# Kernel tuning notes

Measured on AMD Instinct MI355X. Metric: run time of the kernel, lower is better.

The kernel has to match this reference:

```python
import jax, jax.numpy as jnp
import numpy as np

BATCH = 4096
LATENT = 2048
ZDIM = 128
TEMP = 0.5
PRIOR = 0.3
PRIOR_PRIME = 0.5
GAMMA = 1.0
BETA = 0.0
EPS = 1e-8  # torch CosineSimilarity eps


def setup_inputs() -> dict:
    key = jax.random.key(0)
    k = jax.random.split(key, 6)
    return {
        "h_i": jax.random.normal(k[0], (BATCH, LATENT), dtype=jnp.float32),
        "h_j": jax.random.normal(k[1], (BATCH, LATENT), dtype=jnp.float32),
        "z_i": jax.random.normal(k[2], (BATCH, ZDIM), dtype=jnp.float32),
        "z_j": jax.random.normal(k[3], (BATCH, ZDIM), dtype=jnp.float32),
        "target": jax.random.randint(k[4], (BATCH, 1), 0, 2, dtype=jnp.int64 if jax.config.jax_enable_x64 else jnp.int32),
        "W": jax.random.normal(k[5], (1, LATENT), dtype=jnp.float32) * (1.0 / np.sqrt(LATENT)),
        "b": jnp.zeros((1,), dtype=jnp.float32),
        "weight_onnpu": jnp.asarray(0.5, dtype=jnp.float32),
    }


def _onnpu_loss(inp, target):
    # inp: [B, 1] classifier logit; target: [B, 1] in {0, 1} -> {-1, +1}
    t = (target * 2 - 1).astype(inp.dtype)
    positive = (t == 1).astype(inp.dtype)
    unlabeled = (t == -1).astype(inp.dtype)
    one = jnp.asarray(1.0, inp.dtype)
    n_pos = jnp.maximum(one, jnp.sum(positive))
    n_unl = jnp.maximum(one, jnp.sum(unlabeled))
    sig = jax.nn.sigmoid  # loss(x) = sigmoid(-x)
    y_pos = sig(-(positive * inp)) * positive
    y_pos_inv = sig(positive * inp) * positive
    y_unl = sig(unlabeled * inp) * unlabeled
    positive_risk = PRIOR_PRIME / n_pos * jnp.sum(y_pos)
    negative_risk = ((1.0 - PRIOR_PRIME) / (n_unl * (1.0 - PRIOR)) * jnp.sum(y_unl)
                     - (1.0 - PRIOR_PRIME) * PRIOR / (n_pos * (1.0 - PRIOR)) * jnp.sum(y_pos_inv))
    # nnPU correction (nnPU=True, beta=0, gamma=1)
    return jnp.where(negative_risk < -BETA, -GAMMA * negative_risk,
                     positive_risk + negative_risk)


def _nt_xent_loss(z_i, z_j):
    B = z_i.shape[0]
    N = 2 * B
    z = jnp.concatenate([z_i, z_j], axis=0)  # [N, D]
    zn = z / jnp.maximum(jnp.linalg.norm(z, axis=1, keepdims=True), EPS)
    sim = (zn @ zn.T) / TEMP  # [N, N] cosine similarity / temperature
    idx = jnp.arange(N)
    pos = sim[idx, (idx + B) % N]  # positive pair logit per row
    # CE over [positive | all-other-than-self]: denominator is logsumexp over
    # the row with the self-similarity (diagonal) excluded.
    sim_masked = jnp.where(idx[:, None] == idx[None, :], -jnp.inf, sim)
    lse = jax.nn.logsumexp(sim_masked, axis=1)
    return jnp.sum(lse - pos) / N


def reference(h_i, h_j, z_i, z_j, target, W, b, weight_onnpu):
    logit_i = h_i @ W.T + b  # [B, 1]
    logit_j = h_j @ W.T + b
    onnpu_l = 0.5 * (_onnpu_loss(logit_i, target) + _onnpu_loss(logit_j, target))
    nt_xent_l = _nt_xent_loss(z_i, z_j)
    return weight_onnpu * onnpu_l + (1.0 - weight_onnpu) * nt_xent_l
```

## Files before the change

kernel.cpp:

```cpp
#include <hip/hip_runtime.h>

#define BATCH  4096
#define NROWS  8192
#define LATENT 2048
#define ZDIM   128
#define PRIORc       0.3f
#define PRIOR_PRIMEc 0.5f

typedef __attribute__((ext_vector_type(8))) short bf16x8;
typedef __attribute__((ext_vector_type(4))) float f32x4;

__device__ inline unsigned short f2bf_rne(float f) {
    unsigned int u = __float_as_uint(f);
    u = u + 0x7fffu + ((u >> 16) & 1u);
    return (unsigned short)(u >> 16);
}

__device__ inline float wave_reduce_sum(float v) {
#pragma unroll
    for (int m = 1; m < 64; m <<= 1) v += __shfl_xor(v, m, 64);
    return v;
}

__global__ void k_zprep(const float* __restrict__ z_i, const float* __restrict__ z_j,
                        unsigned short* __restrict__ znb, float* __restrict__ pos) {
    int wave = threadIdx.x >> 6, lane = threadIdx.x & 63;
    int r = blockIdx.x * 4 + wave;
    int p = r + BATCH;
    float2 a = ((const float2*)(z_i + (size_t)r * ZDIM))[lane];
    float2 c = ((const float2*)(z_j + (size_t)r * ZDIM))[lane];
    float sa = a.x * a.x + a.y * a.y;
    float sc = c.x * c.x + c.y * c.y;
    float dd = a.x * c.x + a.y * c.y;
    sa = wave_reduce_sum(sa);
    sc = wave_reduce_sum(sc);
    dd = wave_reduce_sum(dd);
    float inva = 1.f / fmaxf(sqrtf(sa), 1e-8f);
    float invc = 1.f / fmaxf(sqrtf(sc), 1e-8f);
    if (lane == 0) {
        float pv = 2.0f * dd * inva * invc;
        pos[r] = pv;
        pos[p] = pv;
    }
    int kt = lane >> 4;
    int q  = (lane >> 2) & 3;
    int j  = (lane & 3) * 2;
    int lrow = q * 16;
    float fa = inva * 1.41421356237f, fc = invc * 1.41421356237f;
    {
        size_t off = ((size_t)((r >> 4) * 4 + kt) * 64 + (lrow + (r & 15))) * 8 + j;
        ushort2 w2; w2.x = f2bf_rne(a.x * fa); w2.y = f2bf_rne(a.y * fa);
        *(ushort2*)(znb + off) = w2;
    }
    {
        size_t off = ((size_t)((p >> 4) * 4 + kt) * 64 + (lrow + (p & 15))) * 8 + j;
        ushort2 w2; w2.x = f2bf_rne(c.x * fc); w2.y = f2bf_rne(c.y * fc);
        *(ushort2*)(znb + off) = w2;
    }
}

__global__ void __launch_bounds__(256, 3) k_mega(
        const unsigned short* __restrict__ znb, float* __restrict__ S_row,
        const float* __restrict__ h_i, const float* __restrict__ h_j,
        const float* __restrict__ W, const float* __restrict__ bb,
        float* __restrict__ logits) {
    int bid = blockIdx.x;
    int lane = threadIdx.x & 63, wave = threadIdx.x >> 6;
    if (bid < 1024) {
        int q = lane >> 4, t = lane & 15;
        int row0 = (bid & 63) * 128 + (wave >> 1) * 64;
        int gA = row0 >> 4;
        const bf16x8* zf = (const bf16x8*)znb;

        bf16x8 a[4][4];
#pragma unroll
        for (int mt = 0; mt < 4; ++mt)
#pragma unroll
            for (int kt = 0; kt < 4; ++kt)
                a[mt][kt] = zf[(size_t)((gA + mt) * 4 + kt) * 64 + lane];

        float s[16];
#pragma unroll
        for (int i = 0; i < 16; ++i) s[i] = 0.f;

        int colbase = (bid >> 6) * 512 + (wave & 1) * 64;
        int cb4 = colbase >> 4;
        bf16x8 b[4];
#pragma unroll
        for (int kt = 0; kt < 4; ++kt)
            b[kt] = zf[(size_t)(cb4 * 4 + kt) * 64 + lane];

#pragma unroll 1
        for (int it = 0; it < 4; ++it) {
#pragma unroll
            for (int nt = 0; nt < 4; ++nt) {
                bf16x8 bn[4];
                if (!(it == 3 && nt == 3)) {
                    int ng = cb4 + (nt == 3 ? (it + 1) * 8 : it * 8 + nt + 1);
#pragma unroll
                    for (int kt = 0; kt < 4; ++kt)
                        bn[kt] = zf[(size_t)(ng * 4 + kt) * 64 + lane];
                }
                f32x4 acc[4];
                f32x4 zero = {0.f, 0.f, 0.f, 0.f};
#pragma unroll
                for (int mt = 0; mt < 4; ++mt) acc[mt] = zero;
#pragma unroll
                for (int kt = 0; kt < 4; ++kt)
#pragma unroll
                    for (int mt = 0; mt < 4; ++mt)
                        acc[mt] = __builtin_amdgcn_mfma_f32_16x16x32_bf16(a[mt][kt], b[kt], acc[mt], 0, 0, 0);
                int gcol = colbase + it * 128 + nt * 16 + t;
#pragma unroll
                for (int mt = 0; mt < 4; ++mt) {
                    int rowb = row0 + mt * 16 + q * 4;
#pragma unroll
                    for (int reg = 0; reg < 4; ++reg) {
                        float e = __expf(acc[mt][reg]);
                        s[mt * 4 + reg] += (rowb + reg == gcol) ? 0.f : e;
                    }
                }
#pragma unroll
                for (int kt = 0; kt < 4; ++kt) b[kt] = bn[kt];
            }
        }
#pragma unroll
        for (int i = 0; i < 16; ++i) {
            float v = s[i];
            v += __shfl_xor(v, 1, 64);
            v += __shfl_xor(v, 2, 64);
            v += __shfl_xor(v, 4, 64);
            v += __shfl_xor(v, 8, 64);
            if (t == 0) atomicAdd(&S_row[row0 + (i >> 2) * 16 + q * 4 + (i & 3)], v);
        }
    } else {
        int r = (bid - 1024) * 4 + wave;
        const float* h = (r < BATCH) ? (h_i + (size_t)r * LATENT)
                                     : (h_j + (size_t)(r - BATCH) * LATENT);
        const float4* h4 = (const float4*)h;
        const float4* w4 = (const float4*)W;
        float s = 0.f;
#pragma unroll
        for (int itr = 0; itr < 8; ++itr) {
            float4 av = h4[itr * 64 + lane];
            float4 wv = w4[itr * 64 + lane];
            s += av.x * wv.x + av.y * wv.y + av.z * wv.z + av.w * wv.w;
        }
        s = wave_reduce_sum(s);
        if (lane == 0) logits[r] = s + bb[0];
    }
}

__global__ void k_final(const float* __restrict__ S_row, const float* __restrict__ pos,
                        const float* __restrict__ logits, const int* __restrict__ target,
                        const float* __restrict__ w_onnpu, float* __restrict__ out) {
    float nt_s = 0.f;
    for (int r = threadIdx.x; r < NROWS; r += 1024)
        nt_s += __logf(S_row[r]) - pos[r];
    float v[8];
#pragma unroll
    for (int i = 0; i < 8; ++i) v[i] = 0.f;
    for (int r = threadIdx.x; r < BATCH; r += 1024) {
        float li = logits[r], lj = logits[BATCH + r];
        bool p = (target[r] == 1);
        float si_n = 1.f / (1.f + __expf(li));
        float si_p = 1.f / (1.f + __expf(-li));
        float sj_n = 1.f / (1.f + __expf(lj));
        float sj_p = 1.f / (1.f + __expf(-lj));
        v[0] += p ? 1.f : 0.f;
        v[1] += p ? 0.f : 1.f;
        v[2] += p ? si_n : 0.f;
        v[3] += p ? si_p : 0.f;
        v[4] += p ? 0.f : si_p;
        v[5] += p ? sj_n : 0.f;
        v[6] += p ? sj_p : 0.f;
        v[7] += p ? 0.f : sj_p;
    }
    __shared__ float red[16][9];
    int wave = threadIdx.x >> 6, lane = threadIdx.x & 63;
    nt_s = wave_reduce_sum(nt_s);
#pragma unroll
    for (int i = 0; i < 8; ++i) v[i] = wave_reduce_sum(v[i]);
    if (lane == 0) {
        red[wave][0] = nt_s;
#pragma unroll
        for (int i = 0; i < 8; ++i) red[wave][1 + i] = v[i];
    }
    __syncthreads();
    if (threadIdx.x == 0) {
        float t[9];
#pragma unroll
        for (int i = 0; i < 9; ++i) {
            float acc = 0.f;
#pragma unroll
            for (int wv = 0; wv < 16; ++wv) acc += red[wv][i];
            t[i] = acc;
        }
        float ntxent = t[0] / (float)NROWS;
        float np = fmaxf(1.f, t[1]), nu = fmaxf(1.f, t[2]);
        float pr_i = PRIOR_PRIMEc / np * t[3];
        float nr_i = (1.f - PRIOR_PRIMEc) / (nu * (1.f - PRIORc)) * t[5]
                   - (1.f - PRIOR_PRIMEc) * PRIORc / (np * (1.f - PRIORc)) * t[4];
        float li_loss = (nr_i < 0.f) ? -nr_i : (pr_i + nr_i);
        float pr_j = PRIOR_PRIMEc / np * t[6];
        float nr_j = (1.f - PRIOR_PRIMEc) / (nu * (1.f - PRIORc)) * t[8]
                   - (1.f - PRIOR_PRIMEc) * PRIORc / (np * (1.f - PRIORc)) * t[7];
        float lj_loss = (nr_j < 0.f) ? -nr_j : (pr_j + nr_j);
        float onnpu = 0.5f * (li_loss + lj_loss);
        float w = w_onnpu[0];
        out[0] = w * onnpu + (1.f - w) * ntxent;
    }
}

extern "C" void kernel_launch(void* const* d_in, const int* in_sizes, int n_in,
                              void* d_out, int out_size, void* d_ws, size_t ws_size,
                              hipStream_t stream) {
    const float* h_i = (const float*)d_in[0];
    const float* h_j = (const float*)d_in[1];
    const float* z_i = (const float*)d_in[2];
    const float* z_j = (const float*)d_in[3];
    const int* target = (const int*)d_in[4];
    const float* W = (const float*)d_in[5];
    const float* b = (const float*)d_in[6];
    const float* w_onnpu = (const float*)d_in[7];

    char* ws = (char*)d_ws;
    unsigned short* znb = (unsigned short*)ws;
    float* S_row  = (float*)(ws + 2097152);
    float* pos    = (float*)(ws + 2097152 + 32768);
    float* logits = (float*)(ws + 2097152 + 65536);
    float* out = (float*)d_out;

    hipMemsetAsync(S_row, 0, 32768, stream);
    k_zprep<<<1024, 256, 0, stream>>>(z_i, z_j, znb, pos);
    k_mega<<<3072, 256, 0, stream>>>(znb, S_row, h_i, h_j, W, b, logits);
    k_final<<<1, 1024, 0, stream>>>(S_row, pos, logits, target, w_onnpu, out);
}
```

Before: 136.2 us.

## Fuse final reduction into main kernel, drop memset, subtract diagonal post-hoc

Removes the separate memset and final kernel. S_row and the completion counter are now zeroed in the prep kernel, and the final reduction runs in whichever block of the main kernel finishes last, detected with an atomic counter. The exp is switched to the hardware exp2 by folding log2(e) into the bf16 normalization scale (ZSCALE), which drops the per-element diagonal compare. The diagonal term is instead precomputed from the rounded bf16 values and subtracted before the log. The h loads become nontemporal. This saves launch overhead and ALU work in the hot loop, at the cost of cancellation error when subtracting the diagonal and an extra atomic plus fence in every block.

```diff
diff --git a/kernel.cpp b/kernel.cpp
--- a/kernel.cpp
+++ b/kernel.cpp
@@ -6,6 +6,7 @@
 #define ZDIM   128
 #define PRIORc       0.3f
 #define PRIOR_PRIMEc 0.5f
+#define ZSCALE 1.6986436f
 
 typedef __attribute__((ext_vector_type(8))) short bf16x8;
 typedef __attribute__((ext_vector_type(4))) float f32x4;
@@ -15,7 +16,9 @@
     u = u + 0x7fffu + ((u >> 16) & 1u);
     return (unsigned short)(u >> 16);
 }
-
+__device__ inline float bf2f(unsigned short h) {
+    return __uint_as_float(((unsigned int)h) << 16);
+}
 __device__ inline float wave_reduce_sum(float v) {
 #pragma unroll
     for (int m = 1; m < 64; m <<= 1) v += __shfl_xor(v, m, 64);
@@ -23,18 +26,21 @@
 }
 
 __global__ void k_zprep(const float* __restrict__ z_i, const float* __restrict__ z_j,
-                        unsigned short* __restrict__ znb, float* __restrict__ pos) {
+                        unsigned short* __restrict__ znb, float* __restrict__ pos,
+                        float* __restrict__ expdiag, float* __restrict__ S_row,
+                        unsigned int* __restrict__ counter) {
+    int gid = blockIdx.x * 256 + threadIdx.x;
+    if (gid < NROWS) S_row[gid] = 0.f;
+    if (gid == 0) *counter = 0u;
+
     int wave = threadIdx.x >> 6, lane = threadIdx.x & 63;
     int r = blockIdx.x * 4 + wave;
     int p = r + BATCH;
     float2 a = ((const float2*)(z_i + (size_t)r * ZDIM))[lane];
     float2 c = ((const float2*)(z_j + (size_t)r * ZDIM))[lane];
-    float sa = a.x * a.x + a.y * a.y;
-    float sc = c.x * c.x + c.y * c.y;
-    float dd = a.x * c.x + a.y * c.y;
-    sa = wave_reduce_sum(sa);
-    sc = wave_reduce_sum(sc);
-    dd = wave_reduce_sum(dd);
+    float sa = wave_reduce_sum(a.x * a.x + a.y * a.y);
+    float sc = wave_reduce_sum(c.x * c.x + c.y * c.y);
+    float dd = wave_reduce_sum(a.x * c.x + a.y * c.y);
     float inva = 1.f / fmaxf(sqrtf(sa), 1e-8f);
     float invc = 1.f / fmaxf(sqrtf(sc), 1e-8f);
     if (lane == 0) {
@@ -46,16 +52,25 @@
     int q  = (lane >> 2) & 3;
     int j  = (lane & 3) * 2;
     int lrow = q * 16;
-    float fa = inva * 1.41421356237f, fc = invc * 1.41421356237f;
+    float fa = inva * ZSCALE, fc = invc * ZSCALE;
+    ushort2 wa, wc;
+    wa.x = f2bf_rne(a.x * fa); wa.y = f2bf_rne(a.y * fa);
+    wc.x = f2bf_rne(c.x * fc); wc.y = f2bf_rne(c.y * fc);
     {
         size_t off = ((size_t)((r >> 4) * 4 + kt) * 64 + (lrow + (r & 15))) * 8 + j;
-        ushort2 w2; w2.x = f2bf_rne(a.x * fa); w2.y = f2bf_rne(a.y * fa);
-        *(ushort2*)(znb + off) = w2;
+        *(ushort2*)(znb + off) = wa;
     }
     {
         size_t off = ((size_t)((p >> 4) * 4 + kt) * 64 + (lrow + (p & 15))) * 8 + j;
-        ushort2 w2; w2.x = f2bf_rne(c.x * fc); w2.y = f2bf_rne(c.y * fc);
-        *(ushort2*)(znb + off) = w2;
+        *(ushort2*)(znb + off) = wc;
+    }
+    float xa = bf2f(wa.x), ya = bf2f(wa.y);
+    float xc = bf2f(wc.x), yc = bf2f(wc.y);
+    float sda = wave_reduce_sum(xa * xa + ya * ya);
+    float sdc = wave_reduce_sum(xc * xc + yc * yc);
+    if (lane == 0) {
+        expdiag[r] = __builtin_amdgcn_exp2f(sda);
+        expdiag[p] = __builtin_amdgcn_exp2f(sdc);
     }
 }
 
@@ -63,7 +78,10 @@
         const unsigned short* __restrict__ znb, float* __restrict__ S_row,
         const float* __restrict__ h_i, const float* __restrict__ h_j,
         const float* __restrict__ W, const float* __restrict__ bb,
-        float* __restrict__ logits) {
+        float* __restrict__ logits, const float* __restrict__ pos,
+        const float* __restrict__ expdiag, const int* __restrict__ target,
+        const float* __restrict__ w_onnpu, unsigned int* __restrict__ counter,
+        float* __restrict__ out) {
     int bid = blockIdx.x;
     int lane = threadIdx.x & 63, wave = threadIdx.x >> 6;
     if (bid < 1024) {
@@ -90,6 +108,7 @@
         for (int kt = 0; kt < 4; ++kt)
             b[kt] = zf[(size_t)(cb4 * 4 + kt) * 64 + lane];
 
+        f32x4 zero = {0.f, 0.f, 0.f, 0.f};
 #pragma unroll 1
         for (int it = 0; it < 4; ++it) {
 #pragma unroll
@@ -102,24 +121,19 @@
                         bn[kt] = zf[(size_t)(ng * 4 + kt) * 64 + lane];
                 }
                 f32x4 acc[4];
-                f32x4 zero = {0.f, 0.f, 0.f, 0.f};
-#pragma unroll
-                for (int mt = 0; mt < 4; ++mt) acc[mt] = zero;
-#pragma unroll
-                for (int kt = 0; kt < 4; ++kt)
+#pragma unroll
+                for (int mt = 0; mt < 4; ++mt)
+                    acc[mt] = __builtin_amdgcn_mfma_f32_16x16x32_bf16(a[mt][0], b[0], zero, 0, 0, 0);
+#pragma unroll
+                for (int kt = 1; kt < 4; ++kt)
 #pragma unroll
                     for (int mt = 0; mt < 4; ++mt)
                         acc[mt] = __builtin_amdgcn_mfma_f32_16x16x32_bf16(a[mt][kt], b[kt], acc[mt], 0, 0, 0);
-                int gcol = colbase + it * 128 + nt * 16 + t;
-#pragma unroll
-                for (int mt = 0; mt < 4; ++mt) {
-                    int rowb = row0 + mt * 16 + q * 4;
-#pragma unroll
-                    for (int reg = 0; reg < 4; ++reg) {
-                        float e = __expf(acc[mt][reg]);
-                        s[mt * 4 + reg] += (rowb + reg == gcol) ? 0.f : e;
-                    }
-                }
+#pragma unroll
+                for (int mt = 0; mt < 4; ++mt)
+#pragma unroll
+                    for (int reg = 0; reg < 4; ++reg)
+                        s[mt * 4 + reg] += __builtin_amdgcn_exp2f(acc[mt][reg]);
 #pragma unroll
                 for (int kt = 0; kt < 4; ++kt) b[kt] = bn[kt];
             }
@@ -137,30 +151,35 @@
         int r = (bid - 1024) * 4 + wave;
         const float* h = (r < BATCH) ? (h_i + (size_t)r * LATENT)
                                      : (h_j + (size_t)(r - BATCH) * LATENT);
-        const float4* h4 = (const float4*)h;
-        const float4* w4 = (const float4*)W;
+        const f32x4* h4 = (const f32x4*)h;
+        const f32x4* w4 = (const f32x4*)W;
         float s = 0.f;
 #pragma unroll
         for (int itr = 0; itr < 8; ++itr) {
-            float4 av = h4[itr * 64 + lane];
-            float4 wv = w4[itr * 64 + lane];
+            f32x4 av = __builtin_nontemporal_load(&h4[itr * 64 + lane]);
+            f32x4 wv = w4[itr * 64 + lane];
             s += av.x * wv.x + av.y * wv.y + av.z * wv.z + av.w * wv.w;
         }
         s = wave_reduce_sum(s);
         if (lane == 0) logits[r] = s + bb[0];
     }
-}
-
-__global__ void k_final(const float* __restrict__ S_row, const float* __restrict__ pos,
-                        const float* __restrict__ logits, const int* __restrict__ target,
-                        const float* __restrict__ w_onnpu, float* __restrict__ out) {
+
+    __shared__ bool is_last;
+    __syncthreads();
+    __threadfence();
+    if (threadIdx.x == 0)
+        is_last = (atomicAdd(counter, 1u) == (unsigned)(gridDim.x - 1));
+    __syncthreads();
+    if (!is_last) return;
+    __threadfence();
+
     float nt_s = 0.f;
-    for (int r = threadIdx.x; r < NROWS; r += 1024)
-        nt_s += __logf(S_row[r]) - pos[r];
+    for (int r = threadIdx.x; r < NROWS; r += 256)
+        nt_s += __logf(S_row[r] - expdiag[r]) - pos[r];
     float v[8];
 #pragma unroll
     for (int i = 0; i < 8; ++i) v[i] = 0.f;
-    for (int r = threadIdx.x; r < BATCH; r += 1024) {
+    for (int r = threadIdx.x; r < BATCH; r += 256) {
         float li = logits[r], lj = logits[BATCH + r];
         bool p = (target[r] == 1);
         float si_n = 1.f / (1.f + __expf(li));
@@ -176,8 +195,7 @@
         v[6] += p ? sj_p : 0.f;
         v[7] += p ? 0.f : sj_p;
     }
-    __shared__ float red[16][9];
-    int wave = threadIdx.x >> 6, lane = threadIdx.x & 63;
+    __shared__ float red[4][9];
     nt_s = wave_reduce_sum(nt_s);
 #pragma unroll
     for (int i = 0; i < 8; ++i) v[i] = wave_reduce_sum(v[i]);
@@ -190,12 +208,8 @@
     if (threadIdx.x == 0) {
         float t[9];
 #pragma unroll
-        for (int i = 0; i < 9; ++i) {
-            float acc = 0.f;
-#pragma unroll
-            for (int wv = 0; wv < 16; ++wv) acc += red[wv][i];
-            t[i] = acc;
-        }
+        for (int i = 0; i < 9; ++i)
+            t[i] = red[0][i] + red[1][i] + red[2][i] + red[3][i];
         float ntxent = t[0] / (float)NROWS;
         float np = fmaxf(1.f, t[1]), nu = fmaxf(1.f, t[2]);
         float pr_i = PRIOR_PRIMEc / np * t[3];
@@ -226,13 +240,14 @@
 
     char* ws = (char*)d_ws;
     unsigned short* znb = (unsigned short*)ws;
-    float* S_row  = (float*)(ws + 2097152);
-    float* pos    = (float*)(ws + 2097152 + 32768);
-    float* logits = (float*)(ws + 2097152 + 65536);
+    float* S_row   = (float*)(ws + 2097152);
+    unsigned int* counter = (unsigned int*)(ws + 2097152 + 32768);
+    float* pos     = (float*)(ws + 2097152 + 32768 + 256);
+    float* logits  = (float*)(ws + 2097152 + 65536 + 256);
+    float* expdiag = (float*)(ws + 2097152 + 98304 + 256);
     float* out = (float*)d_out;
 
-    hipMemsetAsync(S_row, 0, 32768, stream);
-    k_zprep<<<1024, 256, 0, stream>>>(z_i, z_j, znb, pos);
-    k_mega<<<3072, 256, 0, stream>>>(znb, S_row, h_i, h_j, W, b, logits);
-    k_final<<<1, 1024, 0, stream>>>(S_row, pos, logits, target, w_onnpu, out);
-}
+    k_zprep<<<1024, 256, 0, stream>>>(z_i, z_j, znb, pos, expdiag, S_row, counter);
+    k_mega<<<3072, 256, 0, stream>>>(znb, S_row, h_i, h_j, W, b, logits,
+                                     pos, expdiag, target, w_onnpu, counter, out);
+}
```

Result: slower. 519.9 us (+281.8%).
